# Kernel optimization log

Hardware: AMD Instinct MI355X
Metric: run time of the kernel (lower is better)

Reference implementation:

```python
import jax, jax.numpy as jnp
import numpy as np

CAPACITY_FACTOR = 1.25

def setup_inputs() -> dict:
    key = jax.random.key(0)
    ks = jax.random.split(key, 6)
    B, S, D, H, E = 4, 2048, 1024, 2048, 8
    x = jax.random.normal(ks[0], (B, S, D), dtype=jnp.float32)
    Wg = jax.random.normal(ks[1], (D, E), dtype=jnp.float32) / np.float32(np.sqrt(D))
    bg = jnp.zeros((E,), dtype=jnp.float32)
    W1 = jax.random.normal(ks[2], (E, H, D), dtype=jnp.float32) / np.float32(np.sqrt(H))
    W2 = jax.random.normal(ks[3], (E, D, H), dtype=jnp.float32) / np.float32(np.sqrt(D))
    W3 = jax.random.normal(ks[4], (E, D, H), dtype=jnp.float32) / np.float32(np.sqrt(D))
    return {"x": x, "Wg": Wg, "bg": bg, "W1": W1, "W2": W2, "W3": W3, "deterministic": 1}


def reference(x, Wg, bg, W1, W2, W3, deterministic):
    # deterministic=True path: no gate noise, no dropout (rate=0 anyway).
    b, s, d = x.shape
    E = W1.shape[0]
    xt = x.reshape(-1, d)                      # [N, d]
    N = xt.shape[0]
    cap = int(N / E * CAPACITY_FACTOR)

    logits = xt @ Wg + bg                      # [N, E]
    eid = jnp.argmax(logits, axis=1)           # [N] assigned expert (top-1)
    onehot = jax.nn.one_hot(eid, E, dtype=xt.dtype)
    # 0-based arrival position of each token within its expert's queue
    pos = (jnp.sum(jnp.cumsum(onehot, axis=0) * onehot, axis=1)).astype(jnp.int32) - 1
    valid = pos < cap                          # capacity mask (pos >= 0 always)
    slot = jnp.where(valid, pos, cap)          # overflow tokens -> dummy slot `cap`

    # Dispatch: scatter tokens into [E, cap+1, d]; slots unique among valid tokens
    buf = jnp.zeros((E, cap + 1, d), dtype=xt.dtype).at[eid, slot].set(xt)
    binp = buf[:, :cap]                        # [E, cap, d] (dummy slot dropped)

    # Grouped SwiGLU FFN per expert
    h = jax.nn.silu(jnp.einsum('ecd,edh->ech', binp, W2)) * jnp.einsum('ecd,edh->ech', binp, W3)
    bout = jnp.einsum('ech,ehd->ecd', h, W1)   # [E, cap, d]

    # Combine: gather each token's expert output; overflow tokens read zero row
    bout = jnp.concatenate([bout, jnp.zeros((E, 1, d), dtype=bout.dtype)], axis=1)
    eout = bout[eid, slot]                     # [N, d]

    weights = jax.nn.softmax(logits, axis=-1)
    gate_w = jnp.take_along_axis(weights, eid[:, None], axis=1)  # [N, 1]
    out = (gate_w * eout).reshape(b, s, d)
    return out
```

## Files before the change

kernel.cpp:

```cpp
#include <hip/hip_runtime.h>

#define N_TOK 8192
#define D_DIM 1024
#define H_DIM 2048
#define E_NUM 8
#define CAP   1280

typedef __attribute__((ext_vector_type(8))) short bf16x8;
typedef __attribute__((ext_vector_type(4))) float f32x4;

__device__ inline unsigned short f2bf(float f) {
  unsigned u = __float_as_uint(f);
  u += 0x7fffu + ((u >> 16) & 1u);
  return (unsigned short)(u >> 16);
}

#define VMCNT(n) asm volatile("s_waitcnt vmcnt(" #n ")" ::: "memory")
#define BARRIER() asm volatile("s_barrier" ::: "memory")

__global__ __launch_bounds__(256) void transpose_cvt_all(const float* __restrict__ W2,
                                                         const float* __restrict__ W3,
                                                         const float* __restrict__ W1,
                                                         unsigned short* __restrict__ w2t,
                                                         unsigned short* __restrict__ w3t,
                                                         unsigned short* __restrict__ w1t) {
  __shared__ float tile[64][33];
  const int id = blockIdx.x;
  const float* src;
  unsigned short* dst;
  int R, C, bx, by, b;
  if (id < 16384) {
    const int q = id & 8191;
    b = q >> 10;
    const int rem = q & 1023;
    bx = rem & 63;
    by = rem >> 6;
    R = D_DIM; C = H_DIM;
    src = (id < 8192 ? W2 : W3);
    dst = (id < 8192 ? w2t : w3t);
  } else {
    const int q = id - 16384;
    b = q >> 10;
    const int rem = q & 1023;
    bx = rem & 31;
    by = rem >> 5;
    R = H_DIM; C = D_DIM;
    src = W1; dst = w1t;
  }
  src += (size_t)b * R * C;
  dst += (size_t)b * R * C;
  const int c0 = bx * 32, r0 = by * 64;
  const int tx = threadIdx.x & 31, ty = threadIdx.x >> 5;
#pragma unroll
  for (int i = 0; i < 8; ++i)
    tile[ty + i * 8][tx] = src[(size_t)(r0 + ty + i * 8) * C + c0 + tx];
  __syncthreads();
  const int rp = threadIdx.x & 31;
  const int cb = threadIdx.x >> 5;
#pragma unroll
  for (int it = 0; it < 4; ++it) {
    const int c = cb + it * 8;
    unsigned short v[2] = {f2bf(tile[2 * rp][c]), f2bf(tile[2 * rp + 1][c])};
    *reinterpret_cast<unsigned*>(dst + (size_t)(c0 + c) * R + r0 + 2 * rp) =
        *reinterpret_cast<unsigned*>(v);
  }
}

__global__ __launch_bounds__(256) void gate_kernel(const float* __restrict__ x,
                                                   const float* __restrict__ Wg,
                                                   const float* __restrict__ bg,
                                                   int* __restrict__ eid,
                                                   float* __restrict__ gatew) {
  __shared__ float wg[E_NUM][D_DIM];
  const int tid = threadIdx.x;
  for (int i = tid; i < D_DIM * E_NUM; i += 256) {
    int d = i >> 3, e = i & 7;
    wg[e][d] = Wg[i];
  }
  __syncthreads();
  const int w = tid >> 6, l = tid & 63;
  const int t = blockIdx.x * 4 + w;
  const float* xr = x + (size_t)t * D_DIM;
  float acc[8] = {0, 0, 0, 0, 0, 0, 0, 0};
#pragma unroll
  for (int i = 0; i < D_DIM / 64; ++i) {
    float xv = xr[l + 64 * i];
#pragma unroll
    for (int e = 0; e < 8; ++e) acc[e] += xv * wg[e][l + 64 * i];
  }
#pragma unroll
  for (int off = 32; off >= 1; off >>= 1) {
#pragma unroll
    for (int e = 0; e < 8; ++e) acc[e] += __shfl_xor(acc[e], off);
  }
  if (l == 0) {
    float best = -1e30f;
    int bi = 0;
#pragma unroll
    for (int e = 0; e < 8; ++e) {
      acc[e] += bg[e];
      if (acc[e] > best) { best = acc[e]; bi = e; }
    }
    float s = 0.f;
#pragma unroll
    for (int e = 0; e < 8; ++e) s += __expf(acc[e] - best);
    eid[t] = bi;
    gatew[t] = 1.f / s;
  }
}

__global__ __launch_bounds__(512) void scan_kernel(const int* __restrict__ eid,
                                                   int* __restrict__ slot,
                                                   int* __restrict__ tok_of) {
  __shared__ int se[N_TOK];
  const int tid = threadIdx.x;
  for (int i = tid; i < N_TOK; i += 512) se[i] = eid[i];
  for (int i = tid; i < E_NUM * CAP; i += 512) tok_of[i] = -1;
  __syncthreads();
  const int e = tid >> 6;
  const int l = tid & 63;
  const unsigned long long lower = (l == 0) ? 0ull : ((1ull << l) - 1ull);
  int cnt = 0;
  for (int base = 0; base < N_TOK; base += 64) {
    const int t = base + l;
    const bool m = (se[t] == e);
    const unsigned long long bal = __ballot(m);
    if (m) {
      const int rank = cnt + __popcll(bal & lower);
      slot[t] = rank < CAP ? rank : CAP;
      if (rank < CAP) tok_of[e * CAP + rank] = t;
    }
    cnt += __popcll(bal);
  }
}

#define SCAT_BLKS (E_NUM * CAP / 4)
__global__ __launch_bounds__(256) void scatter_zero_kernel(const float* __restrict__ x,
                                                           const int* __restrict__ tok_of,
                                                           const int* __restrict__ slot,
                                                           unsigned short* __restrict__ binp,
                                                           float* __restrict__ out) {
  const int l = threadIdx.x & 63;
  if (blockIdx.x < SCAT_BLKS) {
    const int row = blockIdx.x * 4 + (threadIdx.x >> 6);
    const int t = tok_of[row];
    unsigned short* dst = binp + (size_t)row * D_DIM;
    if (t >= 0) {
      const float* src = x + (size_t)t * D_DIM;
#pragma unroll
      for (int i = 0; i < 4; ++i) {
        const int d = (i * 64 + l) * 4;
        float4 v = *reinterpret_cast<const float4*>(src + d);
        unsigned short r[4] = {f2bf(v.x), f2bf(v.y), f2bf(v.z), f2bf(v.w)};
        *reinterpret_cast<uint2*>(dst + d) = *reinterpret_cast<uint2*>(r);
      }
    } else {
      uint2 z = {0u, 0u};
#pragma unroll
      for (int i = 0; i < 4; ++i) {
        const int d = (i * 64 + l) * 4;
        *reinterpret_cast<uint2*>(dst + d) = z;
      }
    }
  } else {
    const int t = (blockIdx.x - SCAT_BLKS) * 4 + (threadIdx.x >> 6);
    if (slot[t] < CAP) return;
    float4 z = {0.f, 0.f, 0.f, 0.f};
#pragma unroll
    for (int i = 0; i < 4; ++i)
      *reinterpret_cast<float4*>(out + (size_t)t * D_DIM + (i * 64 + l) * 4) = z;
  }
}

#define TILE64 (128 * 64)

__device__ inline void stage_tile(const unsigned short* __restrict__ g, int ldg, int k0,
                                  unsigned short* lds, int w, int l) {
  const int gcol = (l & 7) ^ (l >> 3);
  const unsigned short* gsrc = g + (size_t)(w * 32 + (l >> 3)) * ldg + k0 + gcol * 8;
#pragma unroll
  for (int it = 0; it < 4; ++it) {
    __builtin_amdgcn_global_load_lds(
        (const __attribute__((address_space(1))) unsigned int*)(gsrc + (size_t)(it * 8) * ldg),
        (__attribute__((address_space(3))) unsigned int*)(lds + (w * 32 + it * 8) * 64),
        16, 0, 0);
  }
}

__device__ inline bf16x8 lds_frag(const unsigned short* lds, int row, int c16) {
  return *reinterpret_cast<const bf16x8*>(lds + row * 64 + (c16 ^ (row & 7)) * 8);
}

__global__ __launch_bounds__(256, 2) void ffn1_kernel(const unsigned short* __restrict__ binp,
                                                      const unsigned short* __restrict__ w2t,
                                                      const unsigned short* __restrict__ w3t,
                                                      unsigned short* __restrict__ hbuf) {
  __shared__ unsigned short sA[TILE64], sB2[2][TILE64], sB3[2][TILE64];
  const int id = (blockIdx.x & 7) * 160 + (blockIdx.x >> 3);
  const int e = id / 160;
  const int rem = id - e * 160;
  const int bx = rem / 10;
  const int by = rem - bx * 10;
  const unsigned short* A  = binp + (size_t)e * CAP * D_DIM + (size_t)by * 128 * D_DIM;
  const unsigned short* B2 = w2t + (size_t)e * H_DIM * D_DIM + (size_t)bx * 128 * D_DIM;
  const unsigned short* B3 = w3t + (size_t)e * H_DIM * D_DIM + (size_t)bx * 128 * D_DIM;
  unsigned short* H = hbuf + (size_t)e * CAP * H_DIM;
  const int tid = threadIdx.x;
  const int l = tid & 63;
  const int w = tid >> 6, wr = w >> 1, wc = w & 1;
  f32x4 acc2[4][4] = {};
  f32x4 acc3[4][4] = {};

  stage_tile(B2, D_DIM, 0, sB2[0], w, l);
  stage_tile(B3, D_DIM, 0, sB3[0], w, l);

  const int NT = D_DIM / 64;
  int cur = 0;
  for (int kt = 0; kt < NT; ++kt) {
    stage_tile(A, D_DIM, kt * 64, sA, w, l);
    if (kt + 1 < NT) {
      stage_tile(B2, D_DIM, (kt + 1) * 64, sB2[cur ^ 1], w, l);
      stage_tile(B3, D_DIM, (kt + 1) * 64, sB3[cur ^ 1], w, l);
      VMCNT(8);
    } else {
      VMCNT(0);
    }
    BARRIER();
#pragma unroll
    for (int kk = 0; kk < 2; ++kk) {
      const int c16 = kk * 4 + (l >> 4);
      bf16x8 af[4], b2f[4], b3f[4];
#pragma unroll
      for (int f = 0; f < 4; ++f) {
        af[f]  = lds_frag(sA, wr * 64 + f * 16 + (l & 15), c16);
        b2f[f] = lds_frag(sB2[cur], wc * 64 + f * 16 + (l & 15), c16);
        b3f[f] = lds_frag(sB3[cur], wc * 64 + f * 16 + (l & 15), c16);
      }
#pragma unroll
      for (int fm = 0; fm < 4; ++fm)
#pragma unroll
        for (int fn = 0; fn < 4; ++fn) {
          acc2[fm][fn] = __builtin_amdgcn_mfma_f32_16x16x32_bf16(af[fm], b2f[fn], acc2[fm][fn], 0, 0, 0);
          acc3[fm][fn] = __builtin_amdgcn_mfma_f32_16x16x32_bf16(af[fm], b3f[fn], acc3[fm][fn], 0, 0, 0);
        }
    }
    BARRIER();
    cur ^= 1;
  }

  const int row0 = by * 128 + wr * 64;
  const int col0 = bx * 128 + wc * 64;
#pragma unroll
  for (int fm = 0; fm < 4; ++fm)
#pragma unroll
    for (int fn = 0; fn < 4; ++fn)
#pragma unroll
      for (int j = 0; j < 4; ++j) {
        const int row = row0 + fm * 16 + (l >> 4) * 4 + j;
        const int col = col0 + fn * 16 + (l & 15);
        const float v2 = acc2[fm][fn][j];
        const float v3 = acc3[fm][fn][j];
        const float hv = (v2 / (1.0f + __expf(-v2))) * v3;
        H[(size_t)row * H_DIM + col] = f2bf(hv);
      }
}

__global__ __launch_bounds__(256, 2) void ffn2_kernel(const unsigned short* __restrict__ hbuf,
                                                      const unsigned short* __restrict__ w1t,
                                                      const int* __restrict__ tok_of,
                                                      const float* __restrict__ gatew,
                                                      float* __restrict__ out) {
  __shared__ unsigned short sA[TILE64], sB[2][TILE64];
  const int id = (blockIdx.x & 7) * 80 + (blockIdx.x >> 3);
  const int e = id / 80;
  const int rem = id - e * 80;
  const int bx = rem / 10;
  const int by = rem - bx * 10;
  const unsigned short* A = hbuf + (size_t)e * CAP * H_DIM + (size_t)by * 128 * H_DIM;
  const unsigned short* B = w1t + (size_t)e * D_DIM * H_DIM + (size_t)bx * 128 * H_DIM;
  const int* tok = tok_of + e * CAP;
  const int tid = threadIdx.x;
  const int l = tid & 63;
  const int w = tid >> 6, wr = w >> 1, wc = w & 1;
  f32x4 acc[4][4] = {};

  stage_tile(B, H_DIM, 0, sB[0], w, l);

  const int NT = H_DIM / 64;
  int cur = 0;
  for (int kt = 0; kt < NT; ++kt) {
    stage_tile(A, H_DIM, kt * 64, sA, w, l);
    if (kt + 1 < NT) {
      stage_tile(B, H_DIM, (kt + 1) * 64, sB[cur ^ 1], w, l);
      VMCNT(4);
    } else {
      VMCNT(0);
    }
    BARRIER();
#pragma unroll
    for (int kk = 0; kk < 2; ++kk) {
      const int c16 = kk * 4 + (l >> 4);
      bf16x8 af[4], bfr[4];
#pragma unroll
      for (int f = 0; f < 4; ++f) {
        af[f]  = lds_frag(sA, wr * 64 + f * 16 + (l & 15), c16);
        bfr[f] = lds_frag(sB[cur], wc * 64 + f * 16 + (l & 15), c16);
      }
#pragma unroll
      for (int fm = 0; fm < 4; ++fm)
#pragma unroll
        for (int fn = 0; fn < 4; ++fn)
          acc[fm][fn] = __builtin_amdgcn_mfma_f32_16x16x32_bf16(af[fm], bfr[fn], acc[fm][fn], 0, 0, 0);
    }
    BARRIER();
    cur ^= 1;
  }

  const int row0 = by * 128 + wr * 64;
  const int col0 = bx * 128 + wc * 64;
#pragma unroll
  for (int fm = 0; fm < 4; ++fm)
#pragma unroll
    for (int j = 0; j < 4; ++j) {
      const int row = row0 + fm * 16 + (l >> 4) * 4 + j;
      const int t = tok[row];
      if (t >= 0) {
        const float g = gatew[t];
#pragma unroll
        for (int fn = 0; fn < 4; ++fn) {
          const int col = col0 + fn * 16 + (l & 15);
          out[(size_t)t * D_DIM + col] = g * acc[fm][fn][j];
        }
      }
    }
}

extern "C" void kernel_launch(void* const* d_in, const int* in_sizes, int n_in,
                              void* d_out, int out_size, void* d_ws, size_t ws_size,
                              hipStream_t stream) {
  const float* x  = (const float*)d_in[0];
  const float* Wg = (const float*)d_in[1];
  const float* bg = (const float*)d_in[2];
  const float* W1 = (const float*)d_in[3];
  const float* W2 = (const float*)d_in[4];
  const float* W3 = (const float*)d_in[5];
  float* out = (float*)d_out;

  char* ws = (char*)d_ws;
  unsigned short* w2t = (unsigned short*)ws; ws += (size_t)E_NUM * H_DIM * D_DIM * 2;
  unsigned short* w3t = (unsigned short*)ws; ws += (size_t)E_NUM * H_DIM * D_DIM * 2;
  unsigned short* w1t = (unsigned short*)ws; ws += (size_t)E_NUM * D_DIM * H_DIM * 2;
  unsigned short* binp = (unsigned short*)ws; ws += (size_t)E_NUM * CAP * D_DIM * 2;
  unsigned short* hbuf = (unsigned short*)ws; ws += (size_t)E_NUM * CAP * H_DIM * 2;
  int* eid = (int*)ws;    ws += (size_t)N_TOK * 4;
  float* gw = (float*)ws; ws += (size_t)N_TOK * 4;
  int* slot = (int*)ws;   ws += (size_t)N_TOK * 4;
  int* tok_of = (int*)ws; ws += (size_t)E_NUM * CAP * 4;

  transpose_cvt_all<<<24576, 256, 0, stream>>>(W2, W3, W1, w2t, w3t, w1t);
  gate_kernel<<<N_TOK / 4, 256, 0, stream>>>(x, Wg, bg, eid, gw);
  scan_kernel<<<1, 512, 0, stream>>>(eid, slot, tok_of);
  scatter_zero_kernel<<<SCAT_BLKS + N_TOK / 4, 256, 0, stream>>>(x, tok_of, slot, binp, out);
  ffn1_kernel<<<1280, 256, 0, stream>>>(binp, w2t, w3t, hbuf);
  ffn2_kernel<<<640, 256, 0, stream>>>(hbuf, w1t, tok_of, gw, out);
}
```

Baseline: 237.5 us.

## Skip empty 128-row expert tiles via device-built work list in FFN kernels

The scan kernel now counts how many 128-row tiles each expert actually fills (capped at capacity) and writes a compact work list. Both FFN GEMM kernels index that list, and blocks past the populated count exit early, so tiles made only of empty capacity slots are no longer computed. This drops the block-to-expert interleaving swizzle that was there for cache or CU balance, and the early-exit blocks still launch. It relies on scatter having already zeroed the unused rows, so outputs stay unchanged.

```diff
diff --git a/kernel.cpp b/kernel.cpp
--- a/kernel.cpp
+++ b/kernel.cpp
@@ -111,8 +111,11 @@
 
 __global__ __launch_bounds__(512) void scan_kernel(const int* __restrict__ eid,
                                                    int* __restrict__ slot,
-                                                   int* __restrict__ tok_of) {
+                                                   int* __restrict__ tok_of,
+                                                   int* __restrict__ work,
+                                                   int* __restrict__ nwork) {
   __shared__ int se[N_TOK];
+  __shared__ int nby[E_NUM];
   const int tid = threadIdx.x;
   for (int i = tid; i < N_TOK; i += 512) se[i] = eid[i];
   for (int i = tid; i < E_NUM * CAP; i += 512) tok_of[i] = -1;
@@ -132,6 +135,17 @@
     }
     cnt += __popcll(bal);
   }
+  if (l == 0) {
+    const int c = cnt > CAP ? CAP : cnt;
+    nby[e] = (c + 127) >> 7;
+  }
+  __syncthreads();
+  if (tid == 0) {
+    int n = 0;
+    for (int ee = 0; ee < E_NUM; ++ee)
+      for (int b = 0; b < nby[ee]; ++b) work[n++] = (ee << 4) | b;
+    nwork[0] = n;
+  }
 }
 
 #define SCAT_BLKS (E_NUM * CAP / 4)
@@ -194,13 +208,16 @@
 __global__ __launch_bounds__(256, 2) void ffn1_kernel(const unsigned short* __restrict__ binp,
                                                       const unsigned short* __restrict__ w2t,
                                                       const unsigned short* __restrict__ w3t,
+                                                      const int* __restrict__ work,
+                                                      const int* __restrict__ nwork,
                                                       unsigned short* __restrict__ hbuf) {
   __shared__ unsigned short sA[TILE64], sB2[2][TILE64], sB3[2][TILE64];
-  const int id = (blockIdx.x & 7) * 160 + (blockIdx.x >> 3);
-  const int e = id / 160;
-  const int rem = id - e * 160;
-  const int bx = rem / 10;
-  const int by = rem - bx * 10;
+  const int id = blockIdx.x;
+  if (id >= (nwork[0] << 4)) return;
+  const int item = work[id >> 4];
+  const int e = item >> 4;
+  const int by = item & 15;
+  const int bx = id & 15;
   const unsigned short* A  = binp + (size_t)e * CAP * D_DIM + (size_t)by * 128 * D_DIM;
   const unsigned short* B2 = w2t + (size_t)e * H_DIM * D_DIM + (size_t)bx * 128 * D_DIM;
   const unsigned short* B3 = w3t + (size_t)e * H_DIM * D_DIM + (size_t)bx * 128 * D_DIM;
@@ -269,16 +286,19 @@
                                                       const unsigned short* __restrict__ w1t,
                                                       const int* __restrict__ tok_of,
                                                       const float* __restrict__ gatew,
+                                                      const int* __restrict__ work,
+                                                      const int* __restrict__ nwork,
                                                       float* __restrict__ out) {
   __shared__ unsigned short sA[TILE64], sB[2][TILE64];
-  const int id = (blockIdx.x & 7) * 80 + (blockIdx.x >> 3);
-  const int e = id / 80;
-  const int rem = id - e * 80;
-  const int bx = rem / 10;
-  const int by = rem - bx * 10;
+  const int id = blockIdx.x;
+  if (id >= (nwork[0] << 3)) return;
+  const int item = work[id >> 3];
+  const int e = item >> 4;
+  const int by = item & 15;
+  const int bx = id & 7;
+  const int* tok = tok_of + e * CAP;
   const unsigned short* A = hbuf + (size_t)e * CAP * H_DIM + (size_t)by * 128 * H_DIM;
   const unsigned short* B = w1t + (size_t)e * D_DIM * H_DIM + (size_t)bx * 128 * H_DIM;
-  const int* tok = tok_of + e * CAP;
   const int tid = threadIdx.x;
   const int l = tid & 63;
   const int w = tid >> 6, wr = w >> 1, wc = w & 1;
@@ -356,11 +376,13 @@
   float* gw = (float*)ws; ws += (size_t)N_TOK * 4;
   int* slot = (int*)ws;   ws += (size_t)N_TOK * 4;
   int* tok_of = (int*)ws; ws += (size_t)E_NUM * CAP * 4;
+  int* work = (int*)ws;   ws += 128 * 4;
+  int* nwork = (int*)ws;  ws += 4;
 
   transpose_cvt_all<<<24576, 256, 0, stream>>>(W2, W3, W1, w2t, w3t, w1t);
   gate_kernel<<<N_TOK / 4, 256, 0, stream>>>(x, Wg, bg, eid, gw);
-  scan_kernel<<<1, 512, 0, stream>>>(eid, slot, tok_of);
+  scan_kernel<<<1, 512, 0, stream>>>(eid, slot, tok_of, work, nwork);
   scatter_zero_kernel<<<SCAT_BLKS + N_TOK / 4, 256, 0, stream>>>(x, tok_of, slot, binp, out);
-  ffn1_kernel<<<1280, 256, 0, stream>>>(binp, w2t, w3t, hbuf);
-  ffn2_kernel<<<640, 256, 0, stream>>>(hbuf, w1t, tok_of, gw, out);
-}
+  ffn1_kernel<<<1280, 256, 0, stream>>>(binp, w2t, w3t, work, nwork, hbuf);
+  ffn2_kernel<<<640, 256, 0, stream>>>(hbuf, w1t, tok_of, gw, work, nwork, out);
+}
```

New measurement: 249.0 us. 1.05x slower.
